# Performance work log

Hardware: AMD Instinct MI355X
Metric: run time of the kernel (lower is better)

## Reference

```python
import jax, jax.numpy as jnp
import numpy as np

EMBED = 768
SPAT, TEMP, SYNC, GLOB, NEXP = 128, 64, 32, 64, 6


def _delta(x):
    # delta_i = x_i - x_{i-1}, with delta_0 = 0 (x_0 - x_0)
    x_shift = jnp.concatenate([x[:, :1, :], x[:, :-1, :]], axis=1)
    return x - x_shift


def setup_inputs() -> dict:
    key = jax.random.key(0)
    ks = jax.random.split(key, 13)
    B, S, D = 8, 4096, EMBED
    lim = lambda fan_in: 1.0 / np.sqrt(fan_in)
    u = lambda k, shp, fan_in: jax.random.uniform(k, shp, jnp.float32, -lim(fan_in), lim(fan_in))
    return {
        "x_text": jax.random.normal(ks[0], (B, S, D), jnp.float32),
        "x_au": jax.random.normal(ks[1], (B, S, D), jnp.float32),
        "x_vis": jax.random.normal(ks[2], (B, S, D), jnp.float32),
        "W_spat": u(ks[3], (3 * D, SPAT), 3 * D),
        "b_spat": u(ks[4], (SPAT,), 3 * D),
        "W_temp": u(ks[5], (3 * D, TEMP), 3 * D),
        "b_temp": u(ks[6], (TEMP,), 3 * D),
        "W_sync": u(ks[7], (D, SYNC), D),
        "b_sync": u(ks[8], (SYNC,), D),
        "W_glob": u(ks[9], (SPAT + TEMP + SYNC, GLOB), SPAT + TEMP + SYNC),
        "b_glob": u(ks[10], (GLOB,), SPAT + TEMP + SYNC),
        "W_route": u(ks[11], (SPAT + TEMP + SYNC + GLOB, NEXP), SPAT + TEMP + SYNC + GLOB),
        "b_route": u(ks[12], (NEXP,), SPAT + TEMP + SYNC + GLOB),
    }


def reference(x_text, x_au, x_vis, W_spat, b_spat, W_temp, b_temp,
              W_sync, b_sync, W_glob, b_glob, W_route, b_route):
    B, S, D = x_text.shape
    # local spatial: cat(text, au, vis) @ W_spat  -> (B,S,SPAT)
    spat_in = jnp.concatenate([x_text, x_au, x_vis], axis=-1)
    local_spat = jnp.einsum('bsf,fo->bso', spat_in, W_spat) + b_spat
    # local temporal: cat of first-order deltas -> (B,S,TEMP)
    temp_in = jnp.concatenate([_delta(x_text), _delta(x_au), _delta(x_vis)], axis=-1)
    local_temp = jnp.einsum('bsf,fo->bso', temp_in, W_temp) + b_temp
    # local sync: (au - vis) proj -> (B,S,SYNC)
    local_sync = jnp.einsum('bsf,fo->bso', x_au - x_vis, W_sync) + b_sync
    local_vec = jnp.concatenate([local_spat, local_temp, local_sync], axis=-1)
    # global context: mean over sequence of each local stream, then proj
    global_summary = jnp.mean(local_vec, axis=1)  # == cat of per-stream means
    global_vec = global_summary @ W_glob + b_glob  # (B,GLOB)
    # broadcast-concat + route projection
    glob_exp = jnp.broadcast_to(global_vec[:, None, :], (B, S, global_vec.shape[-1]))
    final_feat = jnp.concatenate([local_vec, glob_exp], axis=-1)
    gate_logits = jnp.einsum('bsf,fo->bso', final_feat, W_route) + b_route
    return gate_logits.reshape(-1, W_route.shape[-1])
```

## Files before the change

kernel.cpp:

```cpp
#include <hip/hip_runtime.h>
#include <hip/hip_bf16.h>

#define DIM 768
#define TD 2304
#define NB 8
#define NS 4096
#define NE 6

typedef __attribute__((ext_vector_type(8))) short bf16x8;
typedef __attribute__((ext_vector_type(4))) float f32x4;

#define OFF_BPK    0
#define OFF_A2F    36864
#define OFF_CB0    50688
#define OFF_ACCSUM 50704
#define OFF_CONSTB 50768
#define OFF_QP2    50832

__device__ __forceinline__ unsigned short f2bf(float f) {
    union { float f; unsigned u; } a; a.f = f;
    unsigned r = a.u + 0x7FFFu + ((a.u >> 16) & 1u);
    return (unsigned short)(r >> 16);
}

__device__ __forceinline__ bf16x8 pack8(float4 a, float4 b) {
    union { bf16x8 v; __hip_bfloat162 h[4]; } u;
    u.h[0] = __float22bfloat162_rn(make_float2(a.x, a.y));
    u.h[1] = __float22bfloat162_rn(make_float2(a.z, a.w));
    u.h[2] = __float22bfloat162_rn(make_float2(b.x, b.y));
    u.h[3] = __float22bfloat162_rn(make_float2(b.z, b.w));
    return u.v;
}

__global__ __launch_bounds__(256) void k_fold(
    const float* __restrict__ Wspat, const float* __restrict__ Wtemp,
    const float* __restrict__ Wsync, const float* __restrict__ Wroute,
    const float* __restrict__ Wglob, const float* __restrict__ bglob,
    const float* __restrict__ broute, const float* __restrict__ bspat,
    const float* __restrict__ btemp, const float* __restrict__ bsync,
    unsigned short* __restrict__ Bpk, float* __restrict__ A2F,
    float* __restrict__ cb0, float* __restrict__ accsum)
{
    __shared__ float lwr[288 * NE];
    __shared__ float lgf[224 * NE];
    const int t = threadIdx.x;
    for (int i = t; i < 288 * NE; i += 256) lwr[i] = Wroute[i];
    __syncthreads();
    if (t < 224) {
        float g[NE] = {0, 0, 0, 0, 0, 0};
        for (int o = 0; o < 64; ++o) {
            const float w = Wglob[t * 64 + o];
            #pragma unroll
            for (int e = 0; e < NE; ++e) g[e] += w * lwr[(224 + o) * NE + e];
        }
        #pragma unroll
        for (int e = 0; e < NE; ++e) lgf[t * NE + e] = g[e];
    }
    __syncthreads();
    if (blockIdx.x == 0) {
        if (t < NE) {
            float a = broute[t];
            for (int o = 0; o < 64; ++o)  a += bglob[o] * lwr[(224 + o) * NE + t];
            for (int o = 0; o < 128; ++o) a += bspat[o] * (lwr[o * NE + t] + lgf[o * NE + t]);
            for (int o = 0; o < 64; ++o)  a += btemp[o] * (lwr[(128 + o) * NE + t] + lgf[(128 + o) * NE + t]);
            for (int o = 0; o < 32; ++o)  a += bsync[o] * (lwr[(192 + o) * NE + t] + lgf[(192 + o) * NE + t]);
            cb0[t] = a;
        }
        if (t >= 128 && t < 192) accsum[t - 128] = 0.f;
    }

    const int d = blockIdx.x * 256 + t;
    const int st = d / DIM, dd = d - st * DIM;

    float p[NE] = {0, 0, 0, 0, 0, 0}, a2[NE] = {0, 0, 0, 0, 0, 0};
    for (int o = 0; o < 64; ++o) {
        const float w = Wtemp[d * 64 + o];
        #pragma unroll
        for (int e = 0; e < NE; ++e) {
            p[e]  += w * lwr[(128 + o) * NE + e];
            a2[e] += w * lgf[(128 + o) * NE + e];
        }
    }
    float qq[NE], a1[NE];
    #pragma unroll
    for (int e = 0; e < NE; ++e) { qq[e] = p[e]; a1[e] = 0.f; }
    for (int o = 0; o < 128; ++o) {
        const float w = Wspat[d * 128 + o];
        #pragma unroll
        for (int e = 0; e < NE; ++e) {
            qq[e] += w * lwr[o * NE + e];
            a1[e] += w * lgf[o * NE + e];
        }
    }
    if (st != 0) {
        const float sg = (st == 1) ? 1.f : -1.f;
        for (int o = 0; o < 32; ++o) {
            const float w = sg * Wsync[dd * 32 + o];
            #pragma unroll
            for (int e = 0; e < NE; ++e) {
                qq[e] += w * lwr[(192 + o) * NE + e];
                a1[e] += w * lgf[(192 + o) * NE + e];
            }
        }
    }
    const int ks = d >> 5, kk = d & 31;
    const int lh = (kk >> 3) * 16, j = kk & 7;
    unsigned short* b0 = Bpk + ks * 1024 + j;
    unsigned short* b1 = b0 + 512;
    #pragma unroll
    for (int e = 0; e < NE; ++e) {
        b0[(lh + e) * 8]     = f2bf(qq[e]);
        b0[(lh + 6 + e) * 8] = f2bf(p[e]);
        b1[(lh + e) * 8]     = f2bf(a1[e]);
        A2F[d * NE + e] = a2[e];
    }
}


#define GLOADX(A0, A1, A2, A3, C) { \
    const int gc_ = khalf * 1152 + (C) * 64; \
    const int st_ = gc_ / DIM; \
    const float* Xp_ = (st_ == 0) ? xt : ((st_ == 1) ? xa : xv); \
    const float* Xr_ = Xp_ + rowoff + (gc_ - st_ * DIM); \
    A0 = *(const float4*)(Xr_);      A1 = *(const float4*)(Xr_ + 4); \
    A2 = *(const float4*)(Xr_ + 32); A3 = *(const float4*)(Xr_ + 36); }

#define BLOAD(C, B00, B01, B10, B11) { \
    const unsigned short* bp = Bpk + ((khalf * 18 + (C)) << 11) + (l << 3); \
    B00 = *(const bf16x8*)(bp); \
    B01 = *(const bf16x8*)(bp + 512); \
    B10 = *(const bf16x8*)(bp + 1024); \
    B11 = *(const bf16x8*)(bp + 1536); }

#define CMPT(A0, A1, A2, A3, B00, B01, B10, B11) { \
    const bf16x8 fA0 = pack8(A0, A1); \
    const bf16x8 fA1 = pack8(A2, A3); \
    acc0 = __builtin_amdgcn_mfma_f32_16x16x32_bf16(fA0, B00, acc0, 0, 0, 0); \
    acc1 = __builtin_amdgcn_mfma_f32_16x16x32_bf16(fA0, B01, acc1, 0, 0, 0); \
    acc0 = __builtin_amdgcn_mfma_f32_16x16x32_bf16(fA1, B10, acc0, 0, 0, 0); \
    acc1 = __builtin_amdgcn_mfma_f32_16x16x32_bf16(fA1, B11, acc1, 0, 0, 0); }

__global__ __launch_bounds__(256, 4) void k_main(
    const float* __restrict__ xt, const float* __restrict__ xa, const float* __restrict__ xv,
    const unsigned short* __restrict__ Bpk, float* __restrict__ accsum,
    float* __restrict__ qp2)
{
    const int t = threadIdx.x;
    const int l = t & 63;
    const int w = t >> 6;
    const int bid = blockIdx.x;
    const int khalf = bid & 1;
    const int rblk = bid >> 1;
    const int rb0 = rblk << 6;
    const int bb = rblk >> 6;

    const int arow = rb0 + w * 16 + (l & 15);
    const size_t rowoff = (size_t)arow * DIM + (l >> 4) * 8;

    f32x4 acc0 = {0.f, 0.f, 0.f, 0.f};
    f32x4 acc1 = {0.f, 0.f, 0.f, 0.f};

    float4 pa0, pa1, pa2, pa3, pb0, pb1, pb2, pb3;
    bf16x8 Ba00, Ba01, Ba10, Ba11, Bb00, Bb01, Bb10, Bb11;

    GLOADX(pa0, pa1, pa2, pa3, 0)
    BLOAD(0, Ba00, Ba01, Ba10, Ba11)
    GLOADX(pb0, pb1, pb2, pb3, 1)
    BLOAD(1, Bb00, Bb01, Bb10, Bb11)

    #pragma unroll 1
    for (int c = 0; c < 16; c += 2) {
        CMPT(pa0, pa1, pa2, pa3, Ba00, Ba01, Ba10, Ba11)
        GLOADX(pa0, pa1, pa2, pa3, c + 2)
        BLOAD(c + 2, Ba00, Ba01, Ba10, Ba11)
        CMPT(pb0, pb1, pb2, pb3, Bb00, Bb01, Bb10, Bb11)
        GLOADX(pb0, pb1, pb2, pb3, c + 3)
        BLOAD(c + 3, Bb00, Bb01, Bb10, Bb11)
    }
    CMPT(pa0, pa1, pa2, pa3, Ba00, Ba01, Ba10, Ba11)
    CMPT(pb0, pb1, pb2, pb3, Bb00, Bb01, Bb10, Bb11)

    const int c_out = l & 15, rgrp = l >> 4;
    float* qph = qp2 + (size_t)khalf * ((size_t)NB * NS * 12);
    if (c_out < 12) {
        const size_t rbase = (size_t)(rb0 + w * 16 + rgrp * 4) * 12 + c_out;
        qph[rbase]      = acc0[0];
        qph[rbase + 12] = acc0[1];
        qph[rbase + 24] = acc0[2];
        qph[rbase + 36] = acc0[3];
    }
    float v = acc1[0] + acc1[1] + acc1[2] + acc1[3];
    v += __shfl_xor(v, 16, 64);
    v += __shfl_xor(v, 32, 64);
    if (rgrp == 0 && c_out < 6)
        atomicAdd(&accsum[bb * NE + c_out], v);
}

__global__ __launch_bounds__(256) void k_const(
    const float* __restrict__ xt, const float* __restrict__ xa, const float* __restrict__ xv,
    const float* __restrict__ accsum, const float* __restrict__ A2F,
    const float* __restrict__ cb0, float* __restrict__ constb)
{
    const int b = blockIdx.x, t = threadIdx.x;
    float acc[NE] = {0, 0, 0, 0, 0, 0};
    for (int f = t; f < TD; f += 256) {
        const int st = f / DIM, dd = f - st * DIM;
        const float* Xp = ((st == 0) ? xt : ((st == 1) ? xa : xv)) + (size_t)b * NS * DIM;
        const float dm = Xp[(size_t)(NS - 1) * DIM + dd] - Xp[dd];
        const float* Ap = A2F + f * NE;
        #pragma unroll
        for (int e = 0; e < NE; ++e) acc[e] += dm * Ap[e];
    }
    #pragma unroll
    for (int e = 0; e < NE; ++e)
        for (int m = 1; m < 64; m <<= 1) acc[e] += __shfl_xor(acc[e], m, 64);
    __shared__ float wred[4][NE];
    if ((t & 63) == 0) {
        #pragma unroll
        for (int e = 0; e < NE; ++e) wred[t >> 6][e] = acc[e];
    }
    __syncthreads();
    if (t < NE) {
        const float inv = 1.f / 4096.f;
        const float dsum = wred[0][t] + wred[1][t] + wred[2][t] + wred[3][t];
        constb[b * NE + t] = cb0[t] + accsum[b * NE + t] * inv + dsum * inv;
    }
}

__global__ __launch_bounds__(256) void k_add(
    const float* __restrict__ qp2, const float* __restrict__ constb, float* __restrict__ out)
{
    const int row = blockIdx.x * 256 + threadIdx.x;
    const int b = row >> 12, s = row & (NS - 1);
    const int rowp = (s == 0) ? row : row - 1;
    const size_t H = (size_t)NB * NS * 12;
    const float* q0 = qp2 + (size_t)row * 12;
    const float* q1 = qp2 + H + (size_t)row * 12;
    const float* p0 = qp2 + (size_t)rowp * 12 + 6;
    const float* p1 = qp2 + H + (size_t)rowp * 12 + 6;
    float* op = out + (size_t)row * NE;
    #pragma unroll
    for (int e = 0; e < NE; ++e)
        op[e] = constb[b * NE + e] + q0[e] + q1[e] - p0[e] - p1[e];
}

extern "C" void kernel_launch(void* const* d_in, const int* in_sizes, int n_in,
                              void* d_out, int out_size, void* d_ws, size_t ws_size,
                              hipStream_t stream)
{
    const float* xt     = (const float*)d_in[0];
    const float* xa     = (const float*)d_in[1];
    const float* xv     = (const float*)d_in[2];
    const float* Wspat  = (const float*)d_in[3];
    const float* bspat  = (const float*)d_in[4];
    const float* Wtemp  = (const float*)d_in[5];
    const float* btemp  = (const float*)d_in[6];
    const float* Wsync  = (const float*)d_in[7];
    const float* bsync  = (const float*)d_in[8];
    const float* Wglob  = (const float*)d_in[9];
    const float* bglob  = (const float*)d_in[10];
    const float* Wroute = (const float*)d_in[11];
    const float* broute = (const float*)d_in[12];
    float* out = (float*)d_out;

    float* ws = (float*)d_ws;
    unsigned short* Bpk = (unsigned short*)(ws + OFF_BPK);
    float* A2F    = ws + OFF_A2F;
    float* cb0    = ws + OFF_CB0;
    float* accsum = ws + OFF_ACCSUM;
    float* constb = ws + OFF_CONSTB;
    float* qp2    = ws + OFF_QP2;

    hipMemsetAsync(Bpk, 0, 73728 * sizeof(unsigned short), stream);
    k_fold<<<9, 256, 0, stream>>>(Wspat, Wtemp, Wsync, Wroute, Wglob, bglob,
                                  broute, bspat, btemp, bsync, Bpk, A2F, cb0, accsum);
    k_main<<<1024, 256, 0, stream>>>(xt, xa, xv, Bpk, accsum, qp2);
    k_const<<<8, 256, 0, stream>>>(xt, xa, xv, accsum, A2F, cb0, constb);
    k_add<<<128, 256, 0, stream>>>(qp2, constb, out);
}
```

Baseline: 114.6 us.

## Stage activation tiles through LDS with async global_load_lds double buffering

Replaces the register-prefetched float4 loads of the activation rows with asynchronous global-to-LDS loads into a swizzled, double-buffered shared tile. Each wave stages its own 16 rows and reads them back with swizzled float4 LDS reads before packing to bf16 for MFMA. Explicit vmcnt waits and scheduling barriers order the transfers. The aim is to cut register pressure and keep more loads in flight, but prefetch depth drops to one chunk ahead and the kernel now uses 32 KB of LDS per block.

Result: no change. 116.5 us (+1.6%).

```diff
diff --git a/kernel.cpp b/kernel.cpp
--- a/kernel.cpp
+++ b/kernel.cpp
@@ -117,13 +117,19 @@
 }
 
 
-#define GLOADX(A0, A1, A2, A3, C) { \
+#define GLDS(SRC, DST) \
+    __builtin_amdgcn_global_load_lds((const __attribute__((address_space(1))) void*)(SRC), \
+                                     (__attribute__((address_space(3))) void*)(DST), 16, 0, 0)
+
+#define STAGE(DB, C) { \
     const int gc_ = khalf * 1152 + (C) * 64; \
     const int st_ = gc_ / DIM; \
     const float* Xp_ = (st_ == 0) ? xt : ((st_ == 1) ? xa : xv); \
-    const float* Xr_ = Xp_ + rowoff + (gc_ - st_ * DIM); \
-    A0 = *(const float4*)(Xr_);      A1 = *(const float4*)(Xr_ + 4); \
-    A2 = *(const float4*)(Xr_ + 32); A3 = *(const float4*)(Xr_ + 36); }
+    const float* base_ = Xp_ + (gc_ - st_ * DIM); \
+    GLDS(base_ + soff0, &smem[(DB) * 4096 + (w * 16 + 0) * 64]); \
+    GLDS(base_ + soff1, &smem[(DB) * 4096 + (w * 16 + 4) * 64]); \
+    GLDS(base_ + soff2, &smem[(DB) * 4096 + (w * 16 + 8) * 64]); \
+    GLDS(base_ + soff3, &smem[(DB) * 4096 + (w * 16 + 12) * 64]); }
 
 #define BLOAD(C, B00, B01, B10, B11) { \
     const unsigned short* bp = Bpk + ((khalf * 18 + (C)) << 11) + (l << 3); \
@@ -132,9 +138,14 @@
     B10 = *(const bf16x8*)(bp + 1024); \
     B11 = *(const bf16x8*)(bp + 1536); }
 
-#define CMPT(A0, A1, A2, A3, B00, B01, B10, B11) { \
-    const bf16x8 fA0 = pack8(A0, A1); \
-    const bf16x8 fA1 = pack8(A2, A3); \
+#define CMPT(DB, B00, B01, B10, B11) { \
+    const float* ab_ = &smem[(DB) * 4096 + aoff]; \
+    const float4 x0a = *(const float4*)(ab_ + u0f); \
+    const float4 x0b = *(const float4*)(ab_ + u0f + 4); \
+    const float4 x1a = *(const float4*)(ab_ + u1f); \
+    const float4 x1b = *(const float4*)(ab_ + u1f + 4); \
+    const bf16x8 fA0 = pack8(x0a, x0b); \
+    const bf16x8 fA1 = pack8(x1a, x1b); \
     acc0 = __builtin_amdgcn_mfma_f32_16x16x32_bf16(fA0, B00, acc0, 0, 0, 0); \
     acc1 = __builtin_amdgcn_mfma_f32_16x16x32_bf16(fA0, B01, acc1, 0, 0, 0); \
     acc0 = __builtin_amdgcn_mfma_f32_16x16x32_bf16(fA1, B10, acc0, 0, 0, 0); \
@@ -145,6 +156,7 @@
     const unsigned short* __restrict__ Bpk, float* __restrict__ accsum,
     float* __restrict__ qp2)
 {
+    __shared__ float smem[2 * 64 * 64];
     const int t = threadIdx.x;
     const int l = t & 63;
     const int w = t >> 6;
@@ -154,31 +166,40 @@
     const int rb0 = rblk << 6;
     const int bb = rblk >> 6;
 
-    const int arow = rb0 + w * 16 + (l & 15);
-    const size_t rowoff = (size_t)arow * DIM + (l >> 4) * 8;
+    const int u = l & 15;
+    const int rsub = l >> 4;
+    const int soff0 = (rb0 + w * 16 + 0  + rsub) * DIM + (u ^ ((( 0 + rsub) & 7) << 1)) * 4;
+    const int soff1 = (rb0 + w * 16 + 4  + rsub) * DIM + (u ^ ((( 4 + rsub) & 7) << 1)) * 4;
+    const int soff2 = (rb0 + w * 16 + 8  + rsub) * DIM + (u ^ ((( 8 + rsub) & 7) << 1)) * 4;
+    const int soff3 = (rb0 + w * 16 + 12 + rsub) * DIM + (u ^ (((12 + rsub) & 7) << 1)) * 4;
+
+    const int h2 = (l >> 4) * 2;
+    const int swzr = ((l & 15) & 7) << 1;
+    const int aoff = (w * 16 + (l & 15)) * 64;
+    const int u0f = ((h2) ^ swzr) * 4;
+    const int u1f = ((8 + h2) ^ swzr) * 4;
 
     f32x4 acc0 = {0.f, 0.f, 0.f, 0.f};
     f32x4 acc1 = {0.f, 0.f, 0.f, 0.f};
-
-    float4 pa0, pa1, pa2, pa3, pb0, pb1, pb2, pb3;
-    bf16x8 Ba00, Ba01, Ba10, Ba11, Bb00, Bb01, Bb10, Bb11;
-
-    GLOADX(pa0, pa1, pa2, pa3, 0)
-    BLOAD(0, Ba00, Ba01, Ba10, Ba11)
-    GLOADX(pb0, pb1, pb2, pb3, 1)
-    BLOAD(1, Bb00, Bb01, Bb10, Bb11)
+    bf16x8 B00, B01, B10, B11;
+
+    STAGE(0, 0)
 
     #pragma unroll 1
-    for (int c = 0; c < 16; c += 2) {
-        CMPT(pa0, pa1, pa2, pa3, Ba00, Ba01, Ba10, Ba11)
-        GLOADX(pa0, pa1, pa2, pa3, c + 2)
-        BLOAD(c + 2, Ba00, Ba01, Ba10, Ba11)
-        CMPT(pb0, pb1, pb2, pb3, Bb00, Bb01, Bb10, Bb11)
-        GLOADX(pb0, pb1, pb2, pb3, c + 3)
-        BLOAD(c + 3, Bb00, Bb01, Bb10, Bb11)
-    }
-    CMPT(pa0, pa1, pa2, pa3, Ba00, Ba01, Ba10, Ba11)
-    CMPT(pb0, pb1, pb2, pb3, Bb00, Bb01, Bb10, Bb11)
+    for (int c = 0; c < 17; ++c) {
+        const int db = c & 1;
+        BLOAD(c, B00, B01, B10, B11)
+        __builtin_amdgcn_sched_barrier(0);
+        STAGE(db ^ 1, c + 1)
+        __builtin_amdgcn_sched_barrier(0);
+        asm volatile("s_waitcnt vmcnt(4)" ::: "memory");
+        __builtin_amdgcn_sched_barrier(0);
+        CMPT(db, B00, B01, B10, B11)
+    }
+    BLOAD(17, B00, B01, B10, B11)
+    asm volatile("s_waitcnt vmcnt(0)" ::: "memory");
+    __builtin_amdgcn_sched_barrier(0);
+    CMPT(1, B00, B01, B10, B11)
 
     const int c_out = l & 15, rgrp = l >> 4;
     float* qph = qp2 + (size_t)khalf * ((size_t)NB * NS * 12);
```
